# Kernel optimization log

Hardware: AMD Instinct MI355X
Metric: run time of the kernel (lower is better)

## Reference

```python
import jax, jax.numpy as jnp
import numpy as np

N, E = 20000, 320000
IN_DIM = OUT_DIM = E_IN = E_OUT = 128
BN_EPS = 1e-5

def _lrelu(x):
    return jnp.where(x >= 0, x, 0.1 * x)

def setup_inputs() -> dict:
    key = jax.random.key(0)
    ks = jax.random.split(key, 12)
    def w(k, shape):
        return jax.random.normal(k, shape, jnp.float32) * (shape[0] ** -0.5)
    return {
        "h": jax.random.normal(ks[0], (N, IN_DIM), jnp.float32),
        "edge_w": jax.random.normal(ks[1], (E, E_IN), jnp.float32),
        "W_node": w(ks[2], (IN_DIM, OUT_DIM)),
        "W_eedge": w(ks[3], (E_IN, E_IN)),
        "W_esf": w(ks[4], (E_IN, 1)),
        "W_fuse": w(ks[5], (2 * OUT_DIM + E_IN, OUT_DIM)),
        "b_fuse": jnp.zeros((OUT_DIM,), jnp.float32),
        "W_attn": w(ks[6], (OUT_DIM, 1)),
        "W_conc": w(ks[7], (2 * OUT_DIM + E_IN, OUT_DIM)),
        "b_conc": jnp.zeros((OUT_DIM,), jnp.float32),
        "bn_gamma": jnp.ones((E_IN,), jnp.float32),
        "bn_beta": jnp.zeros((E_IN,), jnp.float32),
        "W_aggre": w(ks[8], (2 * OUT_DIM + 2 * E_IN, E_OUT)),
        "src": jax.random.randint(ks[9], (E,), 0, N),
        "dst": jax.random.randint(ks[10], (E,), 0, N),
    }

def reference(h, edge_w, W_node, W_eedge, W_esf, W_fuse, b_fuse, W_attn,
              W_conc, b_conc, bn_gamma, bn_beta, W_aggre, src, dst):
    # eval mode: dropout = identity, BatchNorm uses running stats (mean 0, var 1)
    hn = h @ W_node                       # embed_node -> ndata['h'] = ndata['oh']
    # self_attention: ow = embed_edge(w); w = edge_sf_atten(lrelu(ow)) * ow
    ow = edge_w @ W_eedge                 # [E, e_in]
    w1 = (_lrelu(ow) @ W_esf) * ow        # [E, e_in]
    # inter_attention
    hs, hd = hn[src], hn[dst]             # [E, out]
    sat = jnp.concatenate([hs, hd, w1], axis=-1)          # [E, 2*out+e_in]
    inw = _lrelu(sat @ W_fuse + b_fuse)                   # [E, out]
    a = inw @ W_attn                                      # [E, 1]
    w2 = a * w1                                           # edata['w']
    # reduce_func2: segment softmax over incoming edges (grouped by dst)
    s = a[:, 0]
    m = jax.ops.segment_max(s, dst, num_segments=N)
    e = jnp.exp(s - m[dst])
    denom = jax.ops.segment_sum(e, dst, num_segments=N)
    alpha = (e / denom[dst])[:, None]                     # [E, 1]
    t = jnp.concatenate([hs, w2], axis=-1)                # [E, out+e_in]
    h_agg = jax.ops.segment_sum(alpha * t, dst, num_segments=N)  # [N, out+e_in]
    h_new = jnp.concatenate([h_agg, hn], axis=-1) @ W_conc + b_conc
    # DGL only updates nodes that received messages; zero-indegree keep embed_node(h)
    indeg = jax.ops.segment_sum(jnp.ones((E,), jnp.float32), dst, num_segments=N)
    h_out = jnp.where(indeg[:, None] > 0, h_new, hn)      # [N, out]
    # edge_calc: BN(w2) then aggre_embed_edge(cat(src_h, dst_h, bn_w, ow))
    w_bn = (w2 / jnp.sqrt(jnp.float32(1.0) + BN_EPS)) * bn_gamma + bn_beta
    z = jnp.concatenate([h_out[src], h_out[dst], w_bn, ow], axis=-1)
    w_out = z @ W_aggre                                   # [E, e_out]
    return h_out, w_out, sat
```

## Files before the change

kernel.cpp:

```cpp
#include <hip/hip_runtime.h>
#include <hip/hip_bf16.h>

#define TB 256
#define TBM 512
#define BM 64
#define BK 32
#define BN 128
#define ASTR 68
#define MAXD 160

static constexpr int NN = 20000;
static constexpr int NE = 320000;

static constexpr long long OFF_HN   = 0;
static constexpr long long OFF_OW   = 2560000;
static constexpr long long OFF_S    = 43520000;
static constexpr long long OFF_DEN  = 43840000;
static constexpr long long OFF_CUR  = 43860000;
static constexpr long long OFF_HAGG = 43880000;
static constexpr long long OFF_WT   = 49000000;
static constexpr long long WS_FLOATS = 49140000;

static constexpr int U_E = 0;
static constexpr int U_F = 32768;
static constexpr int U_A = 131072;

static constexpr long long OUT_HOUT = 0;
static constexpr long long OUT_WOUT = 2560000;
static constexpr long long OUT_SAT  = 43520000;

typedef __attribute__((ext_vector_type(8))) short s8v;
typedef __attribute__((ext_vector_type(4))) float f32x4;

#define MFMA16(a,b,c) __builtin_amdgcn_mfma_f32_16x16x32_bf16(a,b,c,0,0,0)

__device__ __forceinline__ float lrelu(float x){ return x >= 0.f ? x : 0.1f*x; }

__device__ __forceinline__ void split1(float f, unsigned short& hi, unsigned short& lo){
    __hip_bfloat16 h = __float2bfloat16(f);
    float hf = __bfloat162float(h);
    __hip_bfloat16 l = __float2bfloat16(f - hf);
    hi = __builtin_bit_cast(unsigned short, h);
    lo = __builtin_bit_cast(unsigned short, l);
}
__device__ __forceinline__ void split8(float4 a, float4 b, s8v& hi, s8v& lo){
    float v[8] = {a.x,a.y,a.z,a.w,b.x,b.y,b.z,b.w};
#pragma unroll
    for (int j = 0; j < 8; ++j){
        unsigned short hs, ls;
        split1(v[j], hs, ls);
        hi[j] = (short)hs; lo[j] = (short)ls;
    }
}

__device__ __forceinline__ int lds_a(int row, int g){
    return row*32 + ((g ^ (row & 3)) << 3);
}

__device__ __forceinline__ void store_At(float (*Ast)[ASTR], int k4, int r, float4 v){
    Ast[k4+0][r] = v.x; Ast[k4+1][r] = v.y; Ast[k4+2][r] = v.z; Ast[k4+3][r] = v.w;
}
__device__ __forceinline__ void mm_chunk(const float (*Ast)[ASTR], const float (*Bs)[BN],
                                         int r0, int c0, float acc[4][8]){
#pragma unroll 4
    for (int k = 0; k < BK; ++k){
        const float4 av = *(const float4*)&Ast[k][r0];
        const float4 b0 = *(const float4*)&Bs[k][c0];
        const float4 b1 = *(const float4*)&Bs[k][64 + c0];
        const float a0=av.x, a1=av.y, a2=av.z, a3=av.w;
        const float b[8] = {b0.x,b0.y,b0.z,b0.w,b1.x,b1.y,b1.z,b1.w};
#pragma unroll
        for (int j = 0; j < 8; ++j){
            acc[0][j] = fmaf(a0, b[j], acc[0][j]);
            acc[1][j] = fmaf(a1, b[j], acc[1][j]);
            acc[2][j] = fmaf(a2, b[j], acc[2][j]);
            acc[3][j] = fmaf(a3, b[j], acc[3][j]);
        }
    }
}
__device__ __forceinline__ void load_B(const float* __restrict__ W, int kc,
                                       float (*Bs)[BN], int tid){
#pragma unroll
    for (int p = 0; p < 4; ++p){
        int idx = p*TB + tid;
        int row = idx >> 5;
        int c4  = (idx & 31) << 2;
        *(float4*)&Bs[row][c4] = *(const float4*)&W[(size_t)(kc+row)*BN + c4];
    }
}

__device__ __forceinline__ float blockMax(float v, float* sh4){
#pragma unroll
    for (int m = 32; m; m >>= 1) v = fmaxf(v, __shfl_xor(v, m));
    if ((threadIdx.x & 63) == 0) sh4[threadIdx.x >> 6] = v;
    __syncthreads();
    float r = fmaxf(fmaxf(sh4[0], sh4[1]), fmaxf(sh4[2], sh4[3]));
    __syncthreads();
    return r;
}
__device__ __forceinline__ float blockSum(float v, float* sh4){
#pragma unroll
    for (int m = 32; m; m >>= 1) v += __shfl_xor(v, m);
    if ((threadIdx.x & 63) == 0) sh4[threadIdx.x >> 6] = v;
    __syncthreads();
    float r = sh4[0] + sh4[1] + sh4[2] + sh4[3];
    __syncthreads();
    return r;
}

__global__ __launch_bounds__(TB) void k_prep(const float* __restrict__ We,
                                             const float* __restrict__ Wf,
                                             const float* __restrict__ Wa,
                                             unsigned short* __restrict__ wt,
                                             int* __restrict__ cur){
    int id = blockIdx.x*TB + threadIdx.x;
    if (id < NN) cur[id] = 0;
    unsigned short hs, ls;
    if (id < 16384){
        int n = id >> 7, k = id & 127;
        split1(We[(size_t)k*128 + n], hs, ls);
        wt[U_E + id] = hs; wt[U_E + 16384 + id] = ls;
    } else if (id < 65536){
        int local = id - 16384;
        int n = local / 384, k = local - n*384;
        split1(Wf[(size_t)k*128 + n], hs, ls);
        wt[U_F + local] = hs; wt[U_F + 49152 + local] = ls;
    } else if (id < 131072){
        int local = id - 65536;
        int n = local >> 9, k = local & 511;
        split1(Wa[(size_t)k*128 + n], hs, ls);
        wt[U_A + local] = hs; wt[U_A + 65536 + local] = ls;
    }
}

__global__ __launch_bounds__(TB) void kB_count(const int* __restrict__ dst,
                                               int* __restrict__ cur){
    int e = blockIdx.x*TB + threadIdx.x;
    atomicAdd(&cur[dst[e]], 1);
}
__global__ __launch_bounds__(TB) void kC_scan(int* __restrict__ cur,
                                              int* __restrict__ offs){
    __shared__ int part[TB];
    __shared__ int spre[TB];
    const int tid = threadIdx.x;
    const int CH = (NN + TB - 1) / TB;
    const int base = tid * CH;
    int sum = 0;
    for (int i = 0; i < CH; ++i){ int idx = base + i; if (idx < NN) sum += cur[idx]; }
    part[tid] = sum;
    __syncthreads();
    if (tid == 0){ int r = 0; for (int i = 0; i < TB; ++i){ spre[i] = r; r += part[i]; } }
    __syncthreads();
    int run = spre[tid];
    for (int i = 0; i < CH; ++i){
        int idx = base + i;
        if (idx < NN){ int c = cur[idx]; offs[idx] = run; cur[idx] = run; run += c; }
    }
}
__global__ __launch_bounds__(TB) void kD_scatter(const int* __restrict__ dst,
                                                 int* __restrict__ cur,
                                                 int* __restrict__ eidx){
    int e = blockIdx.x*TB + threadIdx.x;
    int p = atomicAdd(&cur[dst[e]], 1);
    eidx[p] = e;
}

__global__ __launch_bounds__(TB) void k1_hn(const float* __restrict__ h,
                                            const float* __restrict__ Wn,
                                            float* __restrict__ hn){
    __shared__ float Ast[BK][ASTR];
    __shared__ float Bs[BK][BN];
    const int tid = threadIdx.x;
    const int rbase = blockIdx.x * BM;
    const int tc = tid & 15, tr = tid >> 4;
    const int r0 = tr*4, c0 = tc*4;
    float acc[4][8] = {};
    for (int kc = 0; kc < 128; kc += BK){
        __syncthreads();
        {
            int lr = tid >> 3, k4 = (tid & 7) << 2;
#pragma unroll
            for (int p = 0; p < 2; ++p){
                int r = p*32 + lr;
                int rr = rbase + r; if (rr >= NN) rr = NN-1;
                float4 v = *(const float4*)&h[(size_t)rr*128 + kc + k4];
                store_At(Ast, k4, r, v);
            }
        }
        load_B(Wn, kc, Bs, tid);
        __syncthreads();
        mm_chunk(Ast, Bs, r0, c0, acc);
    }
#pragma unroll
    for (int i = 0; i < 4; ++i){
        int rr = rbase + r0 + i;
        if (rr < NN){
            float4 o0 = {acc[i][0],acc[i][1],acc[i][2],acc[i][3]};
            float4 o1 = {acc[i][4],acc[i][5],acc[i][6],acc[i][7]};
            *(float4*)&hn[(size_t)rr*128 + c0] = o0;
            *(float4*)&hn[(size_t)rr*128 + 64 + c0] = o1;
        }
    }
}


__global__ __launch_bounds__(TBM) void k2_mfma(const float* __restrict__ ew,
                                               const unsigned short* __restrict__ wtH,
                                               const unsigned short* __restrict__ wtL,
                                               const float* __restrict__ Wesf,
                                               unsigned short* __restrict__ owH,
                                               unsigned short* __restrict__ owL,
                                               float* __restrict__ sat){
    __shared__ __align__(16) unsigned short Ah[4096], Al[4096], Bh[4096], Bl[4096];
    __shared__ float sEsf[128];
    const int tid = threadIdx.x;
    const long long rbase = (long long)blockIdx.x * 128;
    const int lane = tid & 63, w = tid >> 6;
    const int ls = lane & 15, lg = lane >> 4;
    const int srow = tid >> 2, sg = tid & 3;
    if (tid < 128) sEsf[tid] = Wesf[tid];
    f32x4 acc[8] = {};
    for (int kc = 0; kc < 128; kc += 32){
        __syncthreads();
        {
            int kk = kc + sg*8;
            const float* p = &ew[(rbase + srow)*128 + kk];
            float4 v0 = *(const float4*)p, v1 = *(const float4*)(p+4);
            s8v hi, lo; split8(v0, v1, hi, lo);
            *(s8v*)&Ah[lds_a(srow,sg)] = hi; *(s8v*)&Al[lds_a(srow,sg)] = lo;
            *(s8v*)&Bh[lds_a(srow,sg)] = *(const s8v*)&wtH[srow*128 + kk];
            *(s8v*)&Bl[lds_a(srow,sg)] = *(const s8v*)&wtL[srow*128 + kk];
        }
        __syncthreads();
        s8v ah = *(const s8v*)&Ah[lds_a(w*16 + ls, lg)];
        s8v al = *(const s8v*)&Al[lds_a(w*16 + ls, lg)];
#pragma unroll
        for (int ct = 0; ct < 8; ++ct){
            int c = ct*16 + ls;
            s8v bh = *(const s8v*)&Bh[lds_a(c,lg)];
            s8v bl = *(const s8v*)&Bl[lds_a(c,lg)];
            acc[ct] = MFMA16(ah, bh, acc[ct]);
            acc[ct] = MFMA16(ah, bl, acc[ct]);
            acc[ct] = MFMA16(al, bh, acc[ct]);
        }
    }
#pragma unroll
    for (int reg = 0; reg < 4; ++reg){
        float p = 0.f;
#pragma unroll
        for (int ct = 0; ct < 8; ++ct)
            p += lrelu(acc[ct][reg]) * sEsf[ct*16 + ls];
#pragma unroll
        for (int m = 1; m < 16; m <<= 1) p += __shfl_xor(p, m);
        long long orow = rbase + w*16 + lg*4 + reg;
#pragma unroll
        for (int ct = 0; ct < 8; ++ct){
            float o = acc[ct][reg];
            int col = ct*16 + ls;
            sat[orow*384 + 256 + col] = p * o;
            unsigned short hs_, ls_; split1(o, hs_, ls_);
            owH[orow*128 + col] = hs_;
            owL[orow*128 + col] = ls_;
        }
    }
}

__global__ __launch_bounds__(TBM) void k3_mfma(const float* __restrict__ hn,
                                               const unsigned short* __restrict__ wtH,
                                               const unsigned short* __restrict__ wtL,
                                               const float* __restrict__ bf,
                                               const float* __restrict__ Wattn,
                                               const int* __restrict__ src,
                                               const int* __restrict__ dst,
                                               float* __restrict__ sat,
                                               float* __restrict__ w2,
                                               float* __restrict__ s_ws){
    __shared__ __align__(16) unsigned short Ah[4096], Al[4096], Bh[4096], Bl[4096];
    __shared__ float sBf[128], sAtt[128];
    __shared__ int sSrc[128], sDst[128];
    const int tid = threadIdx.x;
    const long long rbase = (long long)blockIdx.x * 128;
    const int lane = tid & 63, w = tid >> 6;
    const int ls = lane & 15, lg = lane >> 4;
    const int srow = tid >> 2, sg = tid & 3;
    if (tid < 128){
        sBf[tid] = bf[tid]; sAtt[tid] = Wattn[tid];
        sSrc[tid] = src[rbase + tid]; sDst[tid] = dst[rbase + tid];
    }
    f32x4 acc[8] = {};
    for (int kc = 0; kc < 384; kc += 32){
        __syncthreads();
        {
            int kk = kc + sg*8;
            long long e = rbase + srow;
            float4 v0, v1;
            if (kk < 128){
                const float* p = &hn[(size_t)sSrc[srow]*128 + kk];
                v0 = *(const float4*)p; v1 = *(const float4*)(p+4);
                *(float4*)&sat[e*384 + kk] = v0; *(float4*)&sat[e*384 + kk + 4] = v1;
            } else if (kk < 256){
                const float* p = &hn[(size_t)sDst[srow]*128 + (kk-128)];
                v0 = *(const float4*)p; v1 = *(const float4*)(p+4);
                *(float4*)&sat[e*384 + kk] = v0; *(float4*)&sat[e*384 + kk + 4] = v1;
            } else {
                const float* p = &sat[e*384 + kk];
                v0 = *(const float4*)p; v1 = *(const float4*)(p+4);
            }
            s8v hi, lo; split8(v0, v1, hi, lo);
            *(s8v*)&Ah[lds_a(srow,sg)] = hi; *(s8v*)&Al[lds_a(srow,sg)] = lo;
            *(s8v*)&Bh[lds_a(srow,sg)] = *(const s8v*)&wtH[srow*384 + kk];
            *(s8v*)&Bl[lds_a(srow,sg)] = *(const s8v*)&wtL[srow*384 + kk];
        }
        __syncthreads();
        s8v ah = *(const s8v*)&Ah[lds_a(w*16 + ls, lg)];
        s8v al = *(const s8v*)&Al[lds_a(w*16 + ls, lg)];
#pragma unroll
        for (int ct = 0; ct < 8; ++ct){
            int c = ct*16 + ls;
            s8v bh = *(const s8v*)&Bh[lds_a(c,lg)];
            s8v bl = *(const s8v*)&Bl[lds_a(c,lg)];
            acc[ct] = MFMA16(ah, bh, acc[ct]);
            acc[ct] = MFMA16(ah, bl, acc[ct]);
            acc[ct] = MFMA16(al, bh, acc[ct]);
        }
    }
#pragma unroll
    for (int reg = 0; reg < 4; ++reg){
        float p = 0.f;
#pragma unroll
        for (int ct = 0; ct < 8; ++ct){
            int col = ct*16 + ls;
            p += lrelu(acc[ct][reg] + sBf[col]) * sAtt[col];
        }
#pragma unroll
        for (int m = 1; m < 16; m <<= 1) p += __shfl_xor(p, m);
        long long orow = rbase + w*16 + lg*4 + reg;
        if (ls == 0) s_ws[orow] = p;
#pragma unroll
        for (int ct = 0; ct < 8; ++ct){
            int col = ct*16 + ls;
            float w1v = sat[orow*384 + 256 + col];
            w2[orow*128 + col] = p * w1v;
        }
    }
}

__global__ __launch_bounds__(TB) void k5_agg(const float* __restrict__ s,
                                             const float* __restrict__ hn,
                                             const float* __restrict__ w2,
                                             const int* __restrict__ src,
                                             const int* __restrict__ eidx,
                                             const int* __restrict__ offs,
                                             const int* __restrict__ cur,
                                             float* __restrict__ hagg,
                                             float* __restrict__ den){
    __shared__ int   sE[MAXD];
    __shared__ int   sSrc[MAXD];
    __shared__ float sA[MAXD];
    __shared__ float sh4[4];
    const int n = blockIdx.x, tid = threadIdx.x;
    const int start = offs[n];
    const int deg = cur[n] - start;
    for (int i = tid; i < deg && i < MAXD; i += TB) sE[i] = eidx[start+i];
    __syncthreads();
    if (tid == 0 && deg > 1){
        int dd = deg < MAXD ? deg : MAXD;
        for (int i = 1; i < dd; ++i){
            int key = sE[i], j = i-1;
            while (j >= 0 && sE[j] > key){ sE[j+1] = sE[j]; --j; }
            sE[j+1] = key;
        }
    }
    __syncthreads();
    float lm = -3.402823466e38f;
    for (int i = tid; i < deg; i += TB){
        int e = (i < MAXD) ? sE[i] : eidx[start+i];
        lm = fmaxf(lm, s[e]);
    }
    const float m = blockMax(lm, sh4);
    float lsum = 0.f;
    for (int i = tid; i < deg; i += TB){
        int e = (i < MAXD) ? sE[i] : eidx[start+i];
        lsum += expf(s[e] - m);
    }
    const float denom = blockSum(lsum, sh4);
    for (int i = tid; i < deg && i < MAXD; i += TB){
        int e = sE[i];
        sA[i] = expf(s[e] - m) / denom;
        sSrc[i] = src[e];
    }
    __syncthreads();
    float acc = 0.f;
    const bool lo = tid < 128;
    for (int i = 0; i < deg; ++i){
        int e, sI; float a;
        if (i < MAXD){ e = sE[i]; a = sA[i]; sI = sSrc[i]; }
        else { e = eidx[start+i]; a = expf(s[e]-m)/denom; sI = src[e]; }
        float v = lo ? hn[(size_t)sI*128 + tid] : w2[(size_t)e*128 + (tid-128)];
        acc = fmaf(a, v, acc);
    }
    hagg[(size_t)n*256 + tid] = acc;
    if (tid == 0) den[n] = (deg > 0) ? denom : 0.f;
}

__global__ __launch_bounds__(TB) void k6_conc(const float* __restrict__ hagg,
                                              const float* __restrict__ hn,
                                              const float* __restrict__ Wc,
                                              const float* __restrict__ bc,
                                              const float* __restrict__ den,
                                              float* __restrict__ hout){
    __shared__ float Ast[BK][ASTR];
    __shared__ float Bs[BK][BN];
    __shared__ float sBc[BN];
    const int tid = threadIdx.x;
    const int rbase = blockIdx.x * BM;
    const int tc = tid & 15, tr = tid >> 4;
    const int r0 = tr*4, c0 = tc*4;
    if (tid < BN) sBc[tid] = bc[tid];
    float acc[4][8] = {};
    for (int chunk = 0; chunk < 12; ++chunk){
        int kc = chunk * BK;
        __syncthreads();
        {
            int lr = tid >> 3, k4 = (tid & 7) << 2;
#pragma unroll
            for (int p = 0; p < 2; ++p){
                int r = p*32 + lr;
                int rr = rbase + r; if (rr >= NN) rr = NN-1;
                float4 v;
                if (chunk < 8) v = *(const float4*)&hagg[(size_t)rr*256 + kc + k4];
                else           v = *(const float4*)&hn[(size_t)rr*128 + (kc-256) + k4];
                store_At(Ast, k4, r, v);
            }
        }
        load_B(Wc, kc, Bs, tid);
        __syncthreads();
        mm_chunk(Ast, Bs, r0, c0, acc);
    }
#pragma unroll
    for (int i = 0; i < 4; ++i){
        int rr = rbase + r0 + i;
        if (rr >= NN) continue;
        bool keep = den[rr] > 0.f;
        float4 h0 = *(const float4*)&hn[(size_t)rr*128 + c0];
        float4 h1 = *(const float4*)&hn[(size_t)rr*128 + 64 + c0];
        float4 o0, o1;
        o0.x = keep ? acc[i][0] + sBc[c0+0] : h0.x;
        o0.y = keep ? acc[i][1] + sBc[c0+1] : h0.y;
        o0.z = keep ? acc[i][2] + sBc[c0+2] : h0.z;
        o0.w = keep ? acc[i][3] + sBc[c0+3] : h0.w;
        o1.x = keep ? acc[i][4] + sBc[64+c0+0] : h1.x;
        o1.y = keep ? acc[i][5] + sBc[64+c0+1] : h1.y;
        o1.z = keep ? acc[i][6] + sBc[64+c0+2] : h1.z;
        o1.w = keep ? acc[i][7] + sBc[64+c0+3] : h1.w;
        *(float4*)&hout[(size_t)rr*128 + c0] = o0;
        *(float4*)&hout[(size_t)rr*128 + 64 + c0] = o1;
    }
}

__global__ __launch_bounds__(TBM) void k7_mfma(const float* __restrict__ hout,
                                               const unsigned short* __restrict__ owH,
                                               const unsigned short* __restrict__ owL,
                                               const float* __restrict__ gamma,
                                               const float* __restrict__ beta,
                                               const unsigned short* __restrict__ wtH,
                                               const unsigned short* __restrict__ wtL,
                                               const int* __restrict__ src,
                                               const int* __restrict__ dst,
                                               float* __restrict__ w2out){
    __shared__ __align__(16) unsigned short Ah[4096], Al[4096], Bh[4096], Bl[4096];
    __shared__ float sGam[128], sBet[128];
    __shared__ int sSrc[128], sDst[128];
    const int tid = threadIdx.x;
    const long long rbase = (long long)blockIdx.x * 128;
    const int lane = tid & 63, w = tid >> 6;
    const int ls = lane & 15, lg = lane >> 4;
    const int srow = tid >> 2, sg = tid & 3;
    const float ISR = 0.9999950000374997f;
    if (tid < 128){
        sGam[tid] = gamma[tid] * ISR; sBet[tid] = beta[tid];
        sSrc[tid] = src[rbase + tid]; sDst[tid] = dst[rbase + tid];
    }
    f32x4 acc[8] = {};
    for (int kc = 0; kc < 512; kc += 32){
        __syncthreads();
        {
            int kk = kc + sg*8;
            long long e = rbase + srow;
            if (kk < 384){
                float4 v0, v1;
                if (kk < 128){
                    const float* p = &hout[(size_t)sSrc[srow]*128 + kk];
                    v0 = *(const float4*)p; v1 = *(const float4*)(p+4);
                } else if (kk < 256){
                    const float* p = &hout[(size_t)sDst[srow]*128 + (kk-128)];
                    v0 = *(const float4*)p; v1 = *(const float4*)(p+4);
                } else {
                    int cb = kk - 256;
                    const float* p = &w2out[e*128 + cb];
                    v0 = *(const float4*)p; v1 = *(const float4*)(p+4);
                    v0.x = fmaf(v0.x, sGam[cb+0], sBet[cb+0]);
                    v0.y = fmaf(v0.y, sGam[cb+1], sBet[cb+1]);
                    v0.z = fmaf(v0.z, sGam[cb+2], sBet[cb+2]);
                    v0.w = fmaf(v0.w, sGam[cb+3], sBet[cb+3]);
                    v1.x = fmaf(v1.x, sGam[cb+4], sBet[cb+4]);
                    v1.y = fmaf(v1.y, sGam[cb+5], sBet[cb+5]);
                    v1.z = fmaf(v1.z, sGam[cb+6], sBet[cb+6]);
                    v1.w = fmaf(v1.w, sGam[cb+7], sBet[cb+7]);
                }
                s8v hi, lo; split8(v0, v1, hi, lo);
                *(s8v*)&Ah[lds_a(srow,sg)] = hi; *(s8v*)&Al[lds_a(srow,sg)] = lo;
            } else {
                *(s8v*)&Ah[lds_a(srow,sg)] = *(const s8v*)&owH[e*128 + (kk-384)];
                *(s8v*)&Al[lds_a(srow,sg)] = *(const s8v*)&owL[e*128 + (kk-384)];
            }
            *(s8v*)&Bh[lds_a(srow,sg)] = *(const s8v*)&wtH[srow*512 + kk];
            *(s8v*)&Bl[lds_a(srow,sg)] = *(const s8v*)&wtL[srow*512 + kk];
        }
        __syncthreads();
        s8v ah = *(const s8v*)&Ah[lds_a(w*16 + ls, lg)];
        s8v al = *(const s8v*)&Al[lds_a(w*16 + ls, lg)];
#pragma unroll
        for (int ct = 0; ct < 8; ++ct){
            int c = ct*16 + ls;
            s8v bh = *(const s8v*)&Bh[lds_a(c,lg)];
            s8v bl = *(const s8v*)&Bl[lds_a(c,lg)];
            acc[ct] = MFMA16(ah, bh, acc[ct]);
            acc[ct] = MFMA16(ah, bl, acc[ct]);
            acc[ct] = MFMA16(al, bh, acc[ct]);
        }
    }
#pragma unroll
    for (int reg = 0; reg < 4; ++reg){
        long long orow = rbase + w*16 + lg*4 + reg;
#pragma unroll
        for (int ct = 0; ct < 8; ++ct)
            w2out[orow*128 + ct*16 + ls] = acc[ct][reg];
    }
}

extern "C" void kernel_launch(void* const* d_in, const int* in_sizes, int n_in,
                              void* d_out, int out_size, void* d_ws, size_t ws_size,
                              hipStream_t stream){
    (void)in_sizes; (void)n_in; (void)out_size;
    const float* h       = (const float*)d_in[0];
    const float* edge_w  = (const float*)d_in[1];
    const float* W_node  = (const float*)d_in[2];
    const float* W_eedge = (const float*)d_in[3];
    const float* W_esf   = (const float*)d_in[4];
    const float* W_fuse  = (const float*)d_in[5];
    const float* b_fuse  = (const float*)d_in[6];
    const float* W_attn  = (const float*)d_in[7];
    const float* W_conc  = (const float*)d_in[8];
    const float* b_conc  = (const float*)d_in[9];
    const float* gamma   = (const float*)d_in[10];
    const float* beta    = (const float*)d_in[11];
    const float* W_aggre = (const float*)d_in[12];
    const int*   src     = (const int*)d_in[13];
    const int*   dst     = (const int*)d_in[14];

    float* out    = (float*)d_out;
    float* o_hout = out + OUT_HOUT;
    float* o_wout = out + OUT_WOUT;
    float* o_sat  = out + OUT_SAT;

    if (ws_size < (size_t)WS_FLOATS * 4) return;
    float* ws     = (float*)d_ws;
    float* w_hn   = ws + OFF_HN;
    unsigned short* w_owH = (unsigned short*)(ws + OFF_OW);
    unsigned short* w_owL = w_owH + (size_t)NE*128;
    float* w_s    = ws + OFF_S;
    float* w_den  = ws + OFF_DEN;
    int*   w_cur  = (int*)(ws + OFF_CUR);
    float* w_hagg = ws + OFF_HAGG;
    unsigned short* w_wt = (unsigned short*)(ws + OFF_WT);

    int* w_eidx = (int*)o_hout;
    int* w_offs = w_eidx + NE;

    hipLaunchKernelGGL(k_prep,    dim3(131072/TB), dim3(TB), 0, stream,
                       W_eedge, W_fuse, W_aggre, w_wt, w_cur);
    hipLaunchKernelGGL(kB_count,  dim3(NE/TB), dim3(TB), 0, stream, dst, w_cur);
    hipLaunchKernelGGL(kC_scan,   dim3(1), dim3(TB), 0, stream, w_cur, w_offs);
    hipLaunchKernelGGL(kD_scatter,dim3(NE/TB), dim3(TB), 0, stream, dst, w_cur, w_eidx);
    hipLaunchKernelGGL(k1_hn,     dim3((NN+BM-1)/BM), dim3(TB), 0, stream, h, W_node, w_hn);
    hipLaunchKernelGGL(k2_mfma,   dim3(NE/128), dim3(TBM), 0, stream, edge_w,
                       w_wt + U_E, w_wt + U_E + 128*128, W_esf,
                       w_owH, w_owL, o_sat);
    hipLaunchKernelGGL(k3_mfma,   dim3(NE/128), dim3(TBM), 0, stream, w_hn,
                       w_wt + U_F, w_wt + U_F + 128*384, b_fuse, W_attn,
                       src, dst, o_sat, o_wout, w_s);
    hipLaunchKernelGGL(k5_agg,    dim3(NN), dim3(TB), 0, stream, w_s, w_hn, o_wout,
                       src, w_eidx, w_offs, w_cur, w_hagg, w_den);
    hipLaunchKernelGGL(k6_conc,   dim3((NN+BM-1)/BM), dim3(TB), 0, stream, w_hagg, w_hn,
                       W_conc, b_conc, w_den, o_hout);
    hipLaunchKernelGGL(k7_mfma,   dim3(NE/128), dim3(TBM), 0, stream, o_hout,
                       w_owH, w_owL, gamma, beta,
                       w_wt + U_A, w_wt + U_A + 128*512,
                       src, dst, o_wout);
}
```

Measured before the change: 829.9 us.

## Double-buffer MFMA GEMM stages with async global-to-LDS loads and pre-split bf16 node features

The three edge GEMM kernels now double-buffer their LDS tiles, so the next K-chunk is staged while MFMAs run on the current one, with one barrier per iteration instead of two. Weight tiles, and pre-split node and edge operands, are copied straight into LDS with global_load_lds. To make that possible, hn and h_out are stored as pre-split hi/lo bf16 pairs, which removes the split work from the gather loop. The costs are twice the LDS footprint, which may lower occupancy, an h_out hi/lo buffer that reuses the h_agg workspace region, and extra reconstruction adds wherever the fp32 values are needed.

```diff
diff --git a/kernel.cpp b/kernel.cpp
--- a/kernel.cpp
+++ b/kernel.cpp
@@ -31,10 +31,18 @@
 
 typedef __attribute__((ext_vector_type(8))) short s8v;
 typedef __attribute__((ext_vector_type(4))) float f32x4;
+typedef __attribute__((ext_vector_type(8))) unsigned short u16x8;
+typedef __attribute__((ext_vector_type(4))) unsigned short u16x4;
 
 #define MFMA16(a,b,c) __builtin_amdgcn_mfma_f32_16x16x32_bf16(a,b,c,0,0,0)
 
 __device__ __forceinline__ float lrelu(float x){ return x >= 0.f ? x : 0.1f*x; }
+
+__device__ __forceinline__ void gl16(const void* g, void* l){
+    __builtin_amdgcn_global_load_lds(
+        (const __attribute__((address_space(1))) void*)g,
+        (__attribute__((address_space(3))) void*)l, 16, 0, 0);
+}
 
 __device__ __forceinline__ void split1(float f, unsigned short& hi, unsigned short& lo){
     __hip_bfloat16 h = __float2bfloat16(f);
@@ -51,6 +59,9 @@
         split1(v[j], hs, ls);
         hi[j] = (short)hs; lo[j] = (short)ls;
     }
+}
+__device__ __forceinline__ float bfpair(unsigned short h, unsigned short l){
+    return __uint_as_float(((unsigned)h)<<16) + __uint_as_float(((unsigned)l)<<16);
 }
 
 __device__ __forceinline__ int lds_a(int row, int g){
@@ -167,7 +178,8 @@
 
 __global__ __launch_bounds__(TB) void k1_hn(const float* __restrict__ h,
                                             const float* __restrict__ Wn,
-                                            float* __restrict__ hn){
+                                            unsigned short* __restrict__ hnH,
+                                            unsigned short* __restrict__ hnL){
     __shared__ float Ast[BK][ASTR];
     __shared__ float Bs[BK][BN];
     const int tid = threadIdx.x;
@@ -195,10 +207,17 @@
     for (int i = 0; i < 4; ++i){
         int rr = rbase + r0 + i;
         if (rr < NN){
-            float4 o0 = {acc[i][0],acc[i][1],acc[i][2],acc[i][3]};
-            float4 o1 = {acc[i][4],acc[i][5],acc[i][6],acc[i][7]};
-            *(float4*)&hn[(size_t)rr*128 + c0] = o0;
-            *(float4*)&hn[(size_t)rr*128 + 64 + c0] = o1;
+            u16x4 h0, l0, h1, l1;
+#pragma unroll
+            for (int j = 0; j < 4; ++j){
+                unsigned short hs, ls;
+                split1(acc[i][j], hs, ls);   h0[j] = hs; l0[j] = ls;
+                split1(acc[i][4+j], hs, ls); h1[j] = hs; l1[j] = ls;
+            }
+            *(u16x4*)&hnH[(size_t)rr*128 + c0] = h0;
+            *(u16x4*)&hnL[(size_t)rr*128 + c0] = l0;
+            *(u16x4*)&hnH[(size_t)rr*128 + 64 + c0] = h1;
+            *(u16x4*)&hnL[(size_t)rr*128 + 64 + c0] = l1;
         }
     }
 }
@@ -211,38 +230,44 @@
                                                unsigned short* __restrict__ owH,
                                                unsigned short* __restrict__ owL,
                                                float* __restrict__ sat){
-    __shared__ __align__(16) unsigned short Ah[4096], Al[4096], Bh[4096], Bl[4096];
+    __shared__ __align__(16) unsigned short Ah[2][4096], Al[2][4096], Bh[2][4096], Bl[2][4096];
     __shared__ float sEsf[128];
     const int tid = threadIdx.x;
     const long long rbase = (long long)blockIdx.x * 128;
     const int lane = tid & 63, w = tid >> 6;
     const int ls = lane & 15, lg = lane >> 4;
     const int srow = tid >> 2, sg = tid & 3;
+    const int gsw = sg ^ (srow & 3);
+    const int aslot = srow*32 + (gsw << 3);
     if (tid < 128) sEsf[tid] = Wesf[tid];
     f32x4 acc[8] = {};
-    for (int kc = 0; kc < 128; kc += 32){
-        __syncthreads();
-        {
-            int kk = kc + sg*8;
-            const float* p = &ew[(rbase + srow)*128 + kk];
-            float4 v0 = *(const float4*)p, v1 = *(const float4*)(p+4);
-            s8v hi, lo; split8(v0, v1, hi, lo);
-            *(s8v*)&Ah[lds_a(srow,sg)] = hi; *(s8v*)&Al[lds_a(srow,sg)] = lo;
-            *(s8v*)&Bh[lds_a(srow,sg)] = *(const s8v*)&wtH[srow*128 + kk];
-            *(s8v*)&Bl[lds_a(srow,sg)] = *(const s8v*)&wtL[srow*128 + kk];
-        }
-        __syncthreads();
-        s8v ah = *(const s8v*)&Ah[lds_a(w*16 + ls, lg)];
-        s8v al = *(const s8v*)&Al[lds_a(w*16 + ls, lg)];
+    auto stage = [&](int nb, int t){
+        const int kc = t*32;
+        gl16(&wtH[srow*128 + kc + gsw*8], &Bh[nb][w*512]);
+        gl16(&wtL[srow*128 + kc + gsw*8], &Bl[nb][w*512]);
+        const float* p = &ew[(rbase + srow)*128 + kc + sg*8];
+        float4 v0 = *(const float4*)p, v1 = *(const float4*)(p+4);
+        s8v hi, lo; split8(v0, v1, hi, lo);
+        *(s8v*)&Ah[nb][aslot] = hi; *(s8v*)&Al[nb][aslot] = lo;
+    };
+    stage(0, 0);
+    __syncthreads();
+    int cur = 0;
+    for (int t = 0; t < 4; ++t){
+        if (t+1 < 4) stage(cur^1, t+1);
+        s8v ah = *(const s8v*)&Ah[cur][lds_a(w*16 + ls, lg)];
+        s8v al = *(const s8v*)&Al[cur][lds_a(w*16 + ls, lg)];
 #pragma unroll
         for (int ct = 0; ct < 8; ++ct){
             int c = ct*16 + ls;
-            s8v bh = *(const s8v*)&Bh[lds_a(c,lg)];
-            s8v bl = *(const s8v*)&Bl[lds_a(c,lg)];
+            s8v bh = *(const s8v*)&Bh[cur][lds_a(c,lg)];
+            s8v bl = *(const s8v*)&Bl[cur][lds_a(c,lg)];
             acc[ct] = MFMA16(ah, bh, acc[ct]);
             acc[ct] = MFMA16(ah, bl, acc[ct]);
             acc[ct] = MFMA16(al, bh, acc[ct]);
         }
+        __syncthreads();
+        cur ^= 1;
     }
 #pragma unroll
     for (int reg = 0; reg < 4; ++reg){
@@ -265,7 +290,8 @@
     }
 }
 
-__global__ __launch_bounds__(TBM) void k3_mfma(const float* __restrict__ hn,
+__global__ __launch_bounds__(TBM) void k3_mfma(const unsigned short* __restrict__ hnH,
+                                               const unsigned short* __restrict__ hnL,
                                                const unsigned short* __restrict__ wtH,
                                                const unsigned short* __restrict__ wtL,
                                                const float* __restrict__ bf,
@@ -275,7 +301,7 @@
                                                float* __restrict__ sat,
                                                float* __restrict__ w2,
                                                float* __restrict__ s_ws){
-    __shared__ __align__(16) unsigned short Ah[4096], Al[4096], Bh[4096], Bl[4096];
+    __shared__ __align__(16) unsigned short Ah[2][4096], Al[2][4096], Bh[2][4096], Bl[2][4096];
     __shared__ float sBf[128], sAtt[128];
     __shared__ int sSrc[128], sDst[128];
     const int tid = threadIdx.x;
@@ -283,46 +309,59 @@
     const int lane = tid & 63, w = tid >> 6;
     const int ls = lane & 15, lg = lane >> 4;
     const int srow = tid >> 2, sg = tid & 3;
+    const int gsw = sg ^ (srow & 3);
+    const int aslot = srow*32 + (gsw << 3);
     if (tid < 128){
         sBf[tid] = bf[tid]; sAtt[tid] = Wattn[tid];
         sSrc[tid] = src[rbase + tid]; sDst[tid] = dst[rbase + tid];
     }
+    __syncthreads();
     f32x4 acc[8] = {};
-    for (int kc = 0; kc < 384; kc += 32){
-        __syncthreads();
-        {
-            int kk = kc + sg*8;
-            long long e = rbase + srow;
-            float4 v0, v1;
-            if (kk < 128){
-                const float* p = &hn[(size_t)sSrc[srow]*128 + kk];
-                v0 = *(const float4*)p; v1 = *(const float4*)(p+4);
-                *(float4*)&sat[e*384 + kk] = v0; *(float4*)&sat[e*384 + kk + 4] = v1;
-            } else if (kk < 256){
-                const float* p = &hn[(size_t)sDst[srow]*128 + (kk-128)];
-                v0 = *(const float4*)p; v1 = *(const float4*)(p+4);
-                *(float4*)&sat[e*384 + kk] = v0; *(float4*)&sat[e*384 + kk + 4] = v1;
-            } else {
-                const float* p = &sat[e*384 + kk];
-                v0 = *(const float4*)p; v1 = *(const float4*)(p+4);
-            }
+    auto stage = [&](int nb, int t){
+        const int kc = t*32;
+        gl16(&wtH[srow*384 + kc + gsw*8], &Bh[nb][w*512]);
+        gl16(&wtL[srow*384 + kc + gsw*8], &Bl[nb][w*512]);
+        long long e = rbase + srow;
+        if (kc < 256){
+            int node = (kc < 128) ? sSrc[srow] : sDst[srow];
+            int col0 = kc & 127;
+            gl16(&hnH[(size_t)node*128 + col0 + gsw*8], &Ah[nb][w*512]);
+            gl16(&hnL[(size_t)node*128 + col0 + gsw*8], &Al[nb][w*512]);
+            u16x8 hv = *(const u16x8*)&hnH[(size_t)node*128 + col0 + sg*8];
+            u16x8 lv = *(const u16x8*)&hnL[(size_t)node*128 + col0 + sg*8];
+            float f[8];
+#pragma unroll
+            for (int j = 0; j < 8; ++j)
+                f[j] = __uint_as_float(((unsigned)hv[j])<<16)
+                     + __uint_as_float(((unsigned)lv[j])<<16);
+            float4 v0 = {f[0],f[1],f[2],f[3]}, v1 = {f[4],f[5],f[6],f[7]};
+            *(float4*)&sat[e*384 + kc + sg*8] = v0;
+            *(float4*)&sat[e*384 + kc + sg*8 + 4] = v1;
+        } else {
+            const float* p = &sat[e*384 + kc + sg*8];
+            float4 v0 = *(const float4*)p, v1 = *(const float4*)(p+4);
             s8v hi, lo; split8(v0, v1, hi, lo);
-            *(s8v*)&Ah[lds_a(srow,sg)] = hi; *(s8v*)&Al[lds_a(srow,sg)] = lo;
-            *(s8v*)&Bh[lds_a(srow,sg)] = *(const s8v*)&wtH[srow*384 + kk];
-            *(s8v*)&Bl[lds_a(srow,sg)] = *(const s8v*)&wtL[srow*384 + kk];
-        }
-        __syncthreads();
-        s8v ah = *(const s8v*)&Ah[lds_a(w*16 + ls, lg)];
-        s8v al = *(const s8v*)&Al[lds_a(w*16 + ls, lg)];
+            *(s8v*)&Ah[nb][aslot] = hi; *(s8v*)&Al[nb][aslot] = lo;
+        }
+    };
+    stage(0, 0);
+    __syncthreads();
+    int cur = 0;
+    for (int t = 0; t < 12; ++t){
+        if (t+1 < 12) stage(cur^1, t+1);
+        s8v ah = *(const s8v*)&Ah[cur][lds_a(w*16 + ls, lg)];
+        s8v al = *(const s8v*)&Al[cur][lds_a(w*16 + ls, lg)];
 #pragma unroll
         for (int ct = 0; ct < 8; ++ct){
             int c = ct*16 + ls;
-            s8v bh = *(const s8v*)&Bh[lds_a(c,lg)];
-            s8v bl = *(const s8v*)&Bl[lds_a(c,lg)];
+            s8v bh = *(const s8v*)&Bh[cur][lds_a(c,lg)];
+            s8v bl = *(const s8v*)&Bl[cur][lds_a(c,lg)];
             acc[ct] = MFMA16(ah, bh, acc[ct]);
             acc[ct] = MFMA16(ah, bl, acc[ct]);
             acc[ct] = MFMA16(al, bh, acc[ct]);
         }
+        __syncthreads();
+        cur ^= 1;
     }
 #pragma unroll
     for (int reg = 0; reg < 4; ++reg){
@@ -346,7 +385,8 @@
 }
 
 __global__ __launch_bounds__(TB) void k5_agg(const float* __restrict__ s,
-                                             const float* __restrict__ hn,
+                                             const unsigned short* __restrict__ hnH,
+                                             const unsigned short* __restrict__ hnL,
                                              const float* __restrict__ w2,
                                              const int* __restrict__ src,
                                              const int* __restrict__ eidx,
@@ -396,19 +436,22 @@
         int e, sI; float a;
         if (i < MAXD){ e = sE[i]; a = sA[i]; sI = sSrc[i]; }
         else { e = eidx[start+i]; a = expf(s[e]-m)/denom; sI = src[e]; }
-        float v = lo ? hn[(size_t)sI*128 + tid] : w2[(size_t)e*128 + (tid-128)];
+        float v = lo ? bfpair(hnH[(size_t)sI*128 + tid], hnL[(size_t)sI*128 + tid])
+                     : w2[(size_t)e*128 + (tid-128)];
         acc = fmaf(a, v, acc);
     }
     hagg[(size_t)n*256 + tid] = acc;
     if (tid == 0) den[n] = (deg > 0) ? denom : 0.f;
 }
 
-__global__ __launch_bounds__(TB) void k6_conc(const float* __restrict__ hagg,
-                                              const float* __restrict__ hn,
+__global__ __launch_bounds__(TB) void k6_conc(const float* hagg,
+                                              const unsigned short* __restrict__ hnH,
+                                              const unsigned short* __restrict__ hnL,
                                               const float* __restrict__ Wc,
                                               const float* __restrict__ bc,
                                               const float* __restrict__ den,
-                                              float* __restrict__ hout){
+                                              float* __restrict__ hout,
+                                              unsigned short* houtHL){
     __shared__ float Ast[BK][ASTR];
     __shared__ float Bs[BK][BN];
     __shared__ float sBc[BN];
@@ -429,7 +472,13 @@
                 int rr = rbase + r; if (rr >= NN) rr = NN-1;
                 float4 v;
                 if (chunk < 8) v = *(const float4*)&hagg[(size_t)rr*256 + kc + k4];
-                else           v = *(const float4*)&hn[(size_t)rr*128 + (kc-256) + k4];
+                else {
+                    int cb = (kc - 256) + k4;
+                    u16x4 hh = *(const u16x4*)&hnH[(size_t)rr*128 + cb];
+                    u16x4 ll = *(const u16x4*)&hnL[(size_t)rr*128 + cb];
+                    v.x = bfpair(hh[0], ll[0]); v.y = bfpair(hh[1], ll[1]);
+                    v.z = bfpair(hh[2], ll[2]); v.w = bfpair(hh[3], ll[3]);
+                }
                 store_At(Ast, k4, r, v);
             }
         }
@@ -442,23 +491,31 @@
         int rr = rbase + r0 + i;
         if (rr >= NN) continue;
         bool keep = den[rr] > 0.f;
-        float4 h0 = *(const float4*)&hn[(size_t)rr*128 + c0];
-        float4 h1 = *(const float4*)&hn[(size_t)rr*128 + 64 + c0];
-        float4 o0, o1;
-        o0.x = keep ? acc[i][0] + sBc[c0+0] : h0.x;
-        o0.y = keep ? acc[i][1] + sBc[c0+1] : h0.y;
-        o0.z = keep ? acc[i][2] + sBc[c0+2] : h0.z;
-        o0.w = keep ? acc[i][3] + sBc[c0+3] : h0.w;
-        o1.x = keep ? acc[i][4] + sBc[64+c0+0] : h1.x;
-        o1.y = keep ? acc[i][5] + sBc[64+c0+1] : h1.y;
-        o1.z = keep ? acc[i][6] + sBc[64+c0+2] : h1.z;
-        o1.w = keep ? acc[i][7] + sBc[64+c0+3] : h1.w;
+        float o[8];
+#pragma unroll
+        for (int j = 0; j < 8; ++j){
+            int col = (j < 4) ? (c0 + j) : (60 + c0 + j);
+            float fb = bfpair(hnH[(size_t)rr*128 + col], hnL[(size_t)rr*128 + col]);
+            o[j] = keep ? acc[i][j] + sBc[col] : fb;
+        }
+        float4 o0 = {o[0],o[1],o[2],o[3]}, o1 = {o[4],o[5],o[6],o[7]};
         *(float4*)&hout[(size_t)rr*128 + c0] = o0;
         *(float4*)&hout[(size_t)rr*128 + 64 + c0] = o1;
-    }
-}
-
-__global__ __launch_bounds__(TBM) void k7_mfma(const float* __restrict__ hout,
+        u16x4 h0, l0, h1, l1;
+#pragma unroll
+        for (int j = 0; j < 4; ++j){
+            unsigned short hs, ls2;
+            split1(o[j], hs, ls2);   h0[j] = hs; l0[j] = ls2;
+            split1(o[4+j], hs, ls2); h1[j] = hs; l1[j] = ls2;
+        }
+        *(u16x4*)&houtHL[(size_t)rr*512 + c0] = h0;
+        *(u16x4*)&houtHL[(size_t)rr*512 + 128 + c0] = l0;
+        *(u16x4*)&houtHL[(size_t)rr*512 + 64 + c0] = h1;
+        *(u16x4*)&houtHL[(size_t)rr*512 + 128 + 64 + c0] = l1;
+    }
+}
+
+__global__ __launch_bounds__(TBM) void k7_mfma(const unsigned short* __restrict__ houtHL,
                                                const unsigned short* __restrict__ owH,
                                                const unsigned short* __restrict__ owL,
                                                const float* __restrict__ gamma,
@@ -468,7 +525,7 @@
                                                const int* __restrict__ src,
                                                const int* __restrict__ dst,
                                                float* __restrict__ w2out){
-    __shared__ __align__(16) unsigned short Ah[4096], Al[4096], Bh[4096], Bl[4096];
+    __shared__ __align__(16) unsigned short Ah[2][4096], Al[2][4096], Bh[2][4096], Bl[2][4096];
     __shared__ float sGam[128], sBet[128];
     __shared__ int sSrc[128], sDst[128];
     const int tid = threadIdx.x;
@@ -476,59 +533,63 @@
     const int lane = tid & 63, w = tid >> 6;
     const int ls = lane & 15, lg = lane >> 4;
     const int srow = tid >> 2, sg = tid & 3;
+    const int gsw = sg ^ (srow & 3);
+    const int aslot = srow*32 + (gsw << 3);
     const float ISR = 0.9999950000374997f;
     if (tid < 128){
         sGam[tid] = gamma[tid] * ISR; sBet[tid] = beta[tid];
         sSrc[tid] = src[rbase + tid]; sDst[tid] = dst[rbase + tid];
     }
+    __syncthreads();
     f32x4 acc[8] = {};
-    for (int kc = 0; kc < 512; kc += 32){
-        __syncthreads();
-        {
-            int kk = kc + sg*8;
-            long long e = rbase + srow;
-            if (kk < 384){
-                float4 v0, v1;
-                if (kk < 128){
-                    const float* p = &hout[(size_t)sSrc[srow]*128 + kk];
-                    v0 = *(const float4*)p; v1 = *(const float4*)(p+4);
-                } else if (kk < 256){
-                    const float* p = &hout[(size_t)sDst[srow]*128 + (kk-128)];
-                    v0 = *(const float4*)p; v1 = *(const float4*)(p+4);
-                } else {
-                    int cb = kk - 256;
-                    const float* p = &w2out[e*128 + cb];
-                    v0 = *(const float4*)p; v1 = *(const float4*)(p+4);
-                    v0.x = fmaf(v0.x, sGam[cb+0], sBet[cb+0]);
-                    v0.y = fmaf(v0.y, sGam[cb+1], sBet[cb+1]);
-                    v0.z = fmaf(v0.z, sGam[cb+2], sBet[cb+2]);
-                    v0.w = fmaf(v0.w, sGam[cb+3], sBet[cb+3]);
-                    v1.x = fmaf(v1.x, sGam[cb+4], sBet[cb+4]);
-                    v1.y = fmaf(v1.y, sGam[cb+5], sBet[cb+5]);
-                    v1.z = fmaf(v1.z, sGam[cb+6], sBet[cb+6]);
-                    v1.w = fmaf(v1.w, sGam[cb+7], sBet[cb+7]);
-                }
-                s8v hi, lo; split8(v0, v1, hi, lo);
-                *(s8v*)&Ah[lds_a(srow,sg)] = hi; *(s8v*)&Al[lds_a(srow,sg)] = lo;
-            } else {
-                *(s8v*)&Ah[lds_a(srow,sg)] = *(const s8v*)&owH[e*128 + (kk-384)];
-                *(s8v*)&Al[lds_a(srow,sg)] = *(const s8v*)&owL[e*128 + (kk-384)];
-            }
-            *(s8v*)&Bh[lds_a(srow,sg)] = *(const s8v*)&wtH[srow*512 + kk];
-            *(s8v*)&Bl[lds_a(srow,sg)] = *(const s8v*)&wtL[srow*512 + kk];
-        }
-        __syncthreads();
-        s8v ah = *(const s8v*)&Ah[lds_a(w*16 + ls, lg)];
-        s8v al = *(const s8v*)&Al[lds_a(w*16 + ls, lg)];
+    auto stage = [&](int nb, int t){
+        const int kc = t*32;
+        gl16(&wtH[srow*512 + kc + gsw*8], &Bh[nb][w*512]);
+        gl16(&wtL[srow*512 + kc + gsw*8], &Bl[nb][w*512]);
+        long long e = rbase + srow;
+        if (kc < 256){
+            int node = (kc < 128) ? sSrc[srow] : sDst[srow];
+            int col0 = kc & 127;
+            gl16(&houtHL[(size_t)node*512 + col0 + gsw*8], &Ah[nb][w*512]);
+            gl16(&houtHL[(size_t)node*512 + 128 + col0 + gsw*8], &Al[nb][w*512]);
+        } else if (kc < 384){
+            int cb = (kc - 256) + sg*8;
+            const float* p = &w2out[e*128 + cb];
+            float4 v0 = *(const float4*)p, v1 = *(const float4*)(p+4);
+            v0.x = fmaf(v0.x, sGam[cb+0], sBet[cb+0]);
+            v0.y = fmaf(v0.y, sGam[cb+1], sBet[cb+1]);
+            v0.z = fmaf(v0.z, sGam[cb+2], sBet[cb+2]);
+            v0.w = fmaf(v0.w, sGam[cb+3], sBet[cb+3]);
+            v1.x = fmaf(v1.x, sGam[cb+4], sBet[cb+4]);
+            v1.y = fmaf(v1.y, sGam[cb+5], sBet[cb+5]);
+            v1.z = fmaf(v1.z, sGam[cb+6], sBet[cb+6]);
+            v1.w = fmaf(v1.w, sGam[cb+7], sBet[cb+7]);
+            s8v hi, lo; split8(v0, v1, hi, lo);
+            *(s8v*)&Ah[nb][aslot] = hi; *(s8v*)&Al[nb][aslot] = lo;
+        } else {
+            int col0 = kc - 384;
+            gl16(&owH[e*128 + col0 + gsw*8], &Ah[nb][w*512]);
+            gl16(&owL[e*128 + col0 + gsw*8], &Al[nb][w*512]);
+        }
+    };
+    stage(0, 0);
+    __syncthreads();
+    int cur = 0;
+    for (int t = 0; t < 16; ++t){
+        if (t+1 < 16) stage(cur^1, t+1);
+        s8v ah = *(const s8v*)&Ah[cur][lds_a(w*16 + ls, lg)];
+        s8v al = *(const s8v*)&Al[cur][lds_a(w*16 + ls, lg)];
 #pragma unroll
         for (int ct = 0; ct < 8; ++ct){
             int c = ct*16 + ls;
-            s8v bh = *(const s8v*)&Bh[lds_a(c,lg)];
-            s8v bl = *(const s8v*)&Bl[lds_a(c,lg)];
+            s8v bh = *(const s8v*)&Bh[cur][lds_a(c,lg)];
+            s8v bl = *(const s8v*)&Bl[cur][lds_a(c,lg)];
             acc[ct] = MFMA16(ah, bh, acc[ct]);
             acc[ct] = MFMA16(ah, bl, acc[ct]);
             acc[ct] = MFMA16(al, bh, acc[ct]);
         }
+        __syncthreads();
+        cur ^= 1;
     }
 #pragma unroll
     for (int reg = 0; reg < 4; ++reg){
@@ -566,13 +627,15 @@
 
     if (ws_size < (size_t)WS_FLOATS * 4) return;
     float* ws     = (float*)d_ws;
-    float* w_hn   = ws + OFF_HN;
+    unsigned short* w_hnH = (unsigned short*)(ws + OFF_HN);
+    unsigned short* w_hnL = w_hnH + (size_t)NN*128;
     unsigned short* w_owH = (unsigned short*)(ws + OFF_OW);
     unsigned short* w_owL = w_owH + (size_t)NE*128;
     float* w_s    = ws + OFF_S;
     float* w_den  = ws + OFF_DEN;
     int*   w_cur  = (int*)(ws + OFF_CUR);
     float* w_hagg = ws + OFF_HAGG;
+    unsigned short* w_houtHL = (unsigned short*)w_hagg;
     unsigned short* w_wt = (unsigned short*)(ws + OFF_WT);
 
     int* w_eidx = (int*)o_hout;
@@ -583,18 +646,19 @@
     hipLaunchKernelGGL(kB_count,  dim3(NE/TB), dim3(TB), 0, stream, dst, w_cur);
     hipLaunchKernelGGL(kC_scan,   dim3(1), dim3(TB), 0, stream, w_cur, w_offs);
     hipLaunchKernelGGL(kD_scatter,dim3(NE/TB), dim3(TB), 0, stream, dst, w_cur, w_eidx);
-    hipLaunchKernelGGL(k1_hn,     dim3((NN+BM-1)/BM), dim3(TB), 0, stream, h, W_node, w_hn);
+    hipLaunchKernelGGL(k1_hn,     dim3((NN+BM-1)/BM), dim3(TB), 0, stream, h, W_node,
+                       w_hnH, w_hnL);
     hipLaunchKernelGGL(k2_mfma,   dim3(NE/128), dim3(TBM), 0, stream, edge_w,
                        w_wt + U_E, w_wt + U_E + 128*128, W_esf,
                        w_owH, w_owL, o_sat);
-    hipLaunchKernelGGL(k3_mfma,   dim3(NE/128), dim3(TBM), 0, stream, w_hn,
+    hipLaunchKernelGGL(k3_mfma,   dim3(NE/128), dim3(TBM), 0, stream, w_hnH, w_hnL,
                        w_wt + U_F, w_wt + U_F + 128*384, b_fuse, W_attn,
                        src, dst, o_sat, o_wout, w_s);
-    hipLaunchKernelGGL(k5_agg,    dim3(NN), dim3(TB), 0, stream, w_s, w_hn, o_wout,
+    hipLaunchKernelGGL(k5_agg,    dim3(NN), dim3(TB), 0, stream, w_s, w_hnH, w_hnL, o_wout,
                        src, w_eidx, w_offs, w_cur, w_hagg, w_den);
-    hipLaunchKernelGGL(k6_conc,   dim3((NN+BM-1)/BM), dim3(TB), 0, stream, w_hagg, w_hn,
-                       W_conc, b_conc, w_den, o_hout);
-    hipLaunchKernelGGL(k7_mfma,   dim3(NE/128), dim3(TBM), 0, stream, o_hout,
+    hipLaunchKernelGGL(k6_conc,   dim3((NN+BM-1)/BM), dim3(TB), 0, stream, w_hagg,
+                       w_hnH, w_hnL, W_conc, b_conc, w_den, o_hout, w_houtHL);
+    hipLaunchKernelGGL(k7_mfma,   dim3(NE/128), dim3(TBM), 0, stream, w_houtHL,
                        w_owH, w_owL, gamma, beta,
                        w_wt + U_A, w_wt + U_A + 128*512,
                        src, dst, o_wout);
```

Result: no change. 834.4 us (+0.5%).
